# Optimization experiments

Hardware: AMD Instinct MI355X
Metric: run time of the kernel (lower is better)

The kernel has to match this reference:

```python
import jax, jax.numpy as jnp
import numpy as np

N_NODES = 100000
N_EDGES = 1600000
F_IN = 128
HID = 128  # nhid*2
NHID = 64
N_GRAPHS = 512
N_CLASSES = 10
NEG_SLOPE = 0.2  # PyG GATConv default


def setup_inputs() -> dict:
    key = jax.random.key(0)
    ks = jax.random.split(key, 16)
    x = jax.random.normal(ks[0], (N_NODES, F_IN), dtype=jnp.float32)
    edge_index = jax.random.randint(ks[1], (2, N_EDGES), 0, N_NODES, dtype=jnp.int64)
    batch = jnp.sort(jax.random.randint(ks[2], (N_NODES,), 0, N_GRAPHS, dtype=jnp.int64))
    def lin(k, fan_in, shape):
        bound = 1.0 / np.sqrt(fan_in)
        return jax.random.uniform(k, shape, jnp.float32, -bound, bound)
    return {
        "x": x, "edge_index": edge_index, "batch": batch,
        "W1": lin(ks[3], F_IN, (F_IN, HID)),
        "a_src1": lin(ks[4], HID, (HID,)),
        "a_dst1": lin(ks[5], HID, (HID,)),
        "b1": jnp.zeros((HID,), jnp.float32),
        "W2": lin(ks[6], HID, (HID, HID)),
        "a_src2": lin(ks[7], HID, (HID,)),
        "a_dst2": lin(ks[8], HID, (HID,)),
        "b2": jnp.zeros((HID,), jnp.float32),
        "W_fc1": lin(ks[9], HID, (HID, NHID)),
        "b_fc1": lin(ks[10], HID, (NHID,)),
        "W_fc2": lin(ks[11], NHID, (NHID, N_CLASSES)),
        "b_fc2": lin(ks[12], NHID, (N_CLASSES,)),
    }


def gat_conv(x, src, dst, W, a_src, a_dst, b):
    # h = W x ; attention e_ij = LeakyReLU(a_src.h_i + a_dst.h_j), softmax over
    # incoming edges of each destination j, then scatter-add aggregation.
    h = x @ W                                   # [N, H]
    alpha_s = h @ a_src                         # [N]
    alpha_d = h @ a_dst                         # [N]
    e = jax.nn.leaky_relu(alpha_s[src] + alpha_d[dst], NEG_SLOPE)  # [E]
    n = x.shape[0]
    m = jax.ops.segment_max(e, dst, num_segments=n)                # per-dst max
    ex = jnp.exp(e - m[dst])
    denom = jax.ops.segment_sum(ex, dst, num_segments=n)
    alpha = ex / denom[dst]                                        # [E]
    out = jax.ops.segment_sum(alpha[:, None] * h[src], dst, num_segments=n)
    return out + b


def reference(x, edge_index, batch, W1, a_src1, a_dst1, b1,
              W2, a_src2, a_dst2, b2, W_fc1, b_fc1, W_fc2, b_fc2):
    n = x.shape[0]
    # GATConv default add_self_loops=True
    loops = jnp.arange(n, dtype=edge_index.dtype)
    src = jnp.concatenate([edge_index[0], loops])
    dst = jnp.concatenate([edge_index[1], loops])

    h = jax.nn.selu(gat_conv(x, src, dst, W1, a_src1, a_dst1, b1))
    h = jax.nn.selu(gat_conv(h, src, dst, W2, a_src2, a_dst2, b2))

    # global mean pool over graphs
    sums = jax.ops.segment_sum(h, batch, num_segments=N_GRAPHS)
    cnts = jax.ops.segment_sum(jnp.ones((n,), h.dtype), batch, num_segments=N_GRAPHS)
    pooled = jax.nn.selu(sums / jnp.maximum(cnts, 1.0)[:, None])   # [G, H]

    g = jax.nn.selu(pooled @ W_fc1 + b_fc1)
    # dropout p=0.5 is identity in eval mode
    logits = g @ W_fc2 + b_fc2
    return jax.nn.log_softmax(logits, axis=-1)
```

## Files before the change

### kernel.cpp

```cpp
#include <hip/hip_runtime.h>
#include <hip/hip_bf16.h>

#define NEG_SLOPE 0.2f
typedef unsigned int uint32;

#define BSHIFT 9
#define BSIZE 512
#define MAXB 256
#define PCHUNK 4096

typedef __attribute__((ext_vector_type(8))) __bf16 bf16x8;
typedef __attribute__((ext_vector_type(4))) float f32x4;

__device__ __forceinline__ float selu_f(float x) {
    const float a = 1.6732632423543772f, s = 1.0507009873554805f;
    return x > 0.0f ? s * x : s * a * (__expf(x) - 1.0f);
}

__device__ __forceinline__ unsigned short f2bf(float x) {
    uint32 u = __float_as_uint(x);
    uint32 r = (u + 0x7fff + ((u >> 16) & 1)) >> 16;
    return (unsigned short)r;
}
__device__ __forceinline__ float bf_lo(uint32 g) { return __uint_as_float(g << 16); }
__device__ __forceinline__ float bf_hi(uint32 g) { return __uint_as_float(g & 0xffff0000u); }

__global__ __launch_bounds__(256) void prep9(const float* __restrict__ W1,
                                             const float* __restrict__ W2,
                                             unsigned short* __restrict__ Wb,
                                             const int* __restrict__ batch,
                                             int* __restrict__ gstart,
                                             const int* __restrict__ ei,
                                             int* __restrict__ gcnt,
                                             int N, int G, int E, int TOT, int GB) {
    __shared__ int lh[MAXB];
    int b = blockIdx.x, t = threadIdx.x;
    if (b < 2) {
        const float* W = b ? W2 : W1;
        unsigned short* oh = Wb + (size_t)b * 32768;
        unsigned short* ol = oh + 16384;
        for (int d = t; d < 16384; d += 256) {
            int j = d & 7, nn = (d >> 3) & 127, g = d >> 10;
            float v = W[(g * 8 + j) * 128 + nn];
            uint32 hu = f2bf(v);
            float hv = __uint_as_float(hu << 16);
            oh[d] = (unsigned short)hu;
            ol[d] = f2bf(v - hv);
        }
    } else if (b < 2 + GB) {
        int i = (b - 2) * 256 + t;
        if (i < N) {
            int bb = batch[i];
            int bp = (i == 0) ? -1 : batch[i - 1];
            for (int q = bp + 1; q <= bb; ++q) gstart[q] = i;
            if (i == N - 1)
                for (int q = bb + 1; q <= G; ++q) gstart[q] = N;
        }
    } else {
        int hb_ = b - 2 - GB;
        lh[t] = 0;
        __syncthreads();
        int eb = hb_ * PCHUNK;
        #pragma unroll
        for (int k = 0; k < PCHUNK / 256; ++k) {
            int e = eb + k * 256 + t;
            if (e < TOT) {
                int d = (e < E) ? ei[E + e] : e - E;
                atomicAdd(&lh[d >> BSHIFT], 1);
            }
        }
        __syncthreads();
        if (lh[t] > 0) atomicAdd(&gcnt[t], lh[t]);
    }
}

__global__ __launch_bounds__(256) void bucket_scan(const int* __restrict__ gcnt,
                                                   int* __restrict__ bstart,
                                                   int* __restrict__ gcursor, int NB, int TOT) {
    __shared__ int sh[256];
    int t = threadIdx.x;
    int v = (t < NB) ? gcnt[t] : 0;
    sh[t] = v;
    __syncthreads();
    for (int off = 1; off < 256; off <<= 1) {
        int add = (t >= off) ? sh[t - off] : 0;
        __syncthreads();
        sh[t] += add;
        __syncthreads();
    }
    int ex = sh[t] - v;
    if (t < NB) { bstart[t] = ex; gcursor[t] = ex; }
    if (t == 0) bstart[NB] = TOT;
}

__global__ __launch_bounds__(256) void partition_edges(const int* __restrict__ ei,
                                                       int* __restrict__ gcursor,
                                                       uint32* __restrict__ tmp,
                                                       int E, int TOT) {
    __shared__ int lcnt[MAXB];
    __shared__ int lstart[MAXB];
    __shared__ int lcur[MAXB];
    __shared__ int gbase[MAXB];
    __shared__ uint32 staged[PCHUNK];
    __shared__ unsigned char bslot[PCHUNK];
    int t = threadIdx.x;
    int eb = blockIdx.x * PCHUNK;
    int sreg[16], dreg[16];
    #pragma unroll
    for (int k = 0; k < 16; ++k) {
        int e = eb + k * 256 + t;
        if (e < TOT) {
            if (e < E) { sreg[k] = ei[e]; dreg[k] = ei[E + e]; }
            else       { sreg[k] = dreg[k] = e - E; }
        } else dreg[k] = -1;
    }
    lcnt[t] = 0;
    __syncthreads();
    #pragma unroll
    for (int k = 0; k < 16; ++k)
        if (dreg[k] >= 0) atomicAdd(&lcnt[dreg[k] >> BSHIFT], 1);
    __syncthreads();
    int v = lcnt[t];
    lstart[t] = v;
    __syncthreads();
    for (int off = 1; off < 256; off <<= 1) {
        int add = (t >= off) ? lstart[t - off] : 0;
        __syncthreads();
        lstart[t] += add;
        __syncthreads();
    }
    int ex = lstart[t] - v;
    __syncthreads();
    lstart[t] = ex;
    lcur[t] = ex;
    if (v > 0) gbase[t] = atomicAdd(&gcursor[t], v);
    __syncthreads();
    #pragma unroll
    for (int k = 0; k < 16; ++k) {
        int d = dreg[k];
        if (d >= 0) {
            int b = d >> BSHIFT;
            int p = atomicAdd(&lcur[b], 1);
            staged[p] = ((uint32)(d & (BSIZE - 1)) << 17) | (uint32)sreg[k];
            bslot[p] = (unsigned char)b;
        }
    }
    __syncthreads();
    int nvalid = TOT - eb; if (nvalid > PCHUNK) nvalid = PCHUNK;
    for (int i = t; i < nvalid; i += 256) {
        int b = bslot[i];
        tmp[gbase[b] + (i - lstart[b])] = staged[i];
    }
}

__global__ __launch_bounds__(256) void bucket_build(const uint32* __restrict__ tmp,
                                                    const int* __restrict__ bstart,
                                                    int* __restrict__ rowptr,
                                                    int* __restrict__ col,
                                                    int N, int TOT, int NB) {
    __shared__ int cnt[BSIZE];
    __shared__ int sums[256];
    int b = blockIdx.x, t = threadIdx.x;
    int lo = b << BSHIFT;
    int nn = N - lo; if (nn > BSIZE) nn = BSIZE;
    cnt[t] = 0; cnt[t + 256] = 0;
    __syncthreads();
    int ebeg = bstart[b], eend = bstart[b + 1];
    for (int i = ebeg + t; i < eend; i += 256)
        atomicAdd(&cnt[tmp[i] >> 17], 1);
    __syncthreads();
    int c0 = cnt[2 * t], c1 = cnt[2 * t + 1];
    int s2 = c0 + c1;
    sums[t] = s2;
    __syncthreads();
    for (int off = 1; off < 256; off <<= 1) {
        int add = (t >= off) ? sums[t - off] : 0;
        __syncthreads();
        sums[t] += add;
        __syncthreads();
    }
    int ex = sums[t] - s2;
    int st0 = ebeg + ex, st1 = st0 + c0;
    if (2 * t < nn)     rowptr[lo + 2 * t] = st0;
    if (2 * t + 1 < nn) rowptr[lo + 2 * t + 1] = st1;
    cnt[2 * t] = st0; cnt[2 * t + 1] = st1;
    __syncthreads();
    for (int i = ebeg + t; i < eend; i += 256) {
        uint32 u = tmp[i];
        int p = atomicAdd(&cnt[u >> 17], 1);
        col[p] = (int)(u & 0x1FFFFu);
    }
    if (b == NB - 1 && t == 0) rowptr[N] = TOT;
}

__device__ __forceinline__ void gemm_core(const bf16x8 ah[2][4],
                                          const __bf16* Wl,
                                          const float* a_src, const float* a_dst,
                                          uint32* hb, float* as_, float* ad_,
                                          int rbase, int n, int col16, int quad) {
    f32x4 acc[2][8];
    #pragma unroll
    for (int mt = 0; mt < 2; ++mt)
        #pragma unroll
        for (int t = 0; t < 8; ++t) acc[mt][t] = (f32x4)(0.0f);

    #pragma unroll
    for (int c = 0; c < 4; ++c) {
        #pragma unroll
        for (int t = 0; t < 8; ++t) {
            int off = (((c * 4 + quad) * 128) + t * 16 + col16) * 8;
            bf16x8 bh = *(const bf16x8*)&Wl[off];
            bf16x8 bl = *(const bf16x8*)&Wl[16384 + off];
            #pragma unroll
            for (int mt = 0; mt < 2; ++mt) {
                acc[mt][t] = __builtin_amdgcn_mfma_f32_16x16x32_bf16(ah[mt][c], bh, acc[mt][t], 0, 0, 0);
                acc[mt][t] = __builtin_amdgcn_mfma_f32_16x16x32_bf16(ah[mt][c], bl, acc[mt][t], 0, 0, 0);
            }
        }
    }
    float asv[8], adv[8];
    #pragma unroll
    for (int t = 0; t < 8; ++t) { asv[t] = a_src[t * 16 + col16]; adv[t] = a_dst[t * 16 + col16]; }
    #pragma unroll
    for (int mt = 0; mt < 2; ++mt) {
        #pragma unroll
        for (int reg = 0; reg < 4; ++reg) {
            float s = 0.0f, d = 0.0f;
            #pragma unroll
            for (int t = 0; t < 8; ++t) {
                float v = acc[mt][t][reg];
                s += v * asv[t]; d += v * adv[t];
            }
            #pragma unroll
            for (int off = 1; off < 16; off <<= 1) {
                s += __shfl_xor(s, off);
                d += __shfl_xor(d, off);
            }
            int r = rbase + mt * 16 + quad * 4 + reg;
            if (col16 == 0 && r < n) { as_[r] = s; ad_[r] = d; }
        }
    }
    #pragma unroll
    for (int mt = 0; mt < 2; ++mt)
    #pragma unroll
    for (int t = 0; t < 8; ++t)
    #pragma unroll
    for (int reg = 0; reg < 4; ++reg) {
        float v = acc[mt][t][reg];
        float p = __shfl_xor(v, 1);
        int r = rbase + mt * 16 + quad * 4 + reg;
        if (!(col16 & 1) && r < n) {
            uint32 pk = (uint32)f2bf(v) | ((uint32)f2bf(p) << 16);
            hb[(size_t)r * 64 + t * 8 + (col16 >> 1)] = pk;
        }
    }
}

__global__ __launch_bounds__(256) void gemm_mfma_f32(const float* __restrict__ X,
                                                     const unsigned short* __restrict__ Wbh,
                                                     const float* __restrict__ a_src,
                                                     const float* __restrict__ a_dst,
                                                     uint32* __restrict__ hb,
                                                     float* __restrict__ as_,
                                                     float* __restrict__ ad_, int n) {
    __shared__ __bf16 Wl[32768];
    const int tid = threadIdx.x;
    {
        const uint4* sw = (const uint4*)Wbh;
        uint4* dw = (uint4*)Wl;
        for (int i = tid; i < 4096; i += 256) dw[i] = sw[i];
    }
    const int lane = tid & 63, wid = tid >> 6;
    const int col16 = lane & 15, quad = lane >> 4;
    const int rbase = blockIdx.x * 128 + wid * 32;
    bf16x8 ah[2][4];
    #pragma unroll
    for (int mt = 0; mt < 2; ++mt) {
        int r = rbase + mt * 16 + col16;
        bool ok = (r < n);
        const float* xp = X + (size_t)r * 128;
        #pragma unroll
        for (int c = 0; c < 4; ++c) {
            int k0 = c * 32 + quad * 8;
            float4 x0 = ok ? *(const float4*)(xp + k0)     : make_float4(0.f,0.f,0.f,0.f);
            float4 x1 = ok ? *(const float4*)(xp + k0 + 4) : make_float4(0.f,0.f,0.f,0.f);
            float xs[8] = {x0.x,x0.y,x0.z,x0.w,x1.x,x1.y,x1.z,x1.w};
            #pragma unroll
            for (int j = 0; j < 8; ++j) ah[mt][c][j] = (__bf16)xs[j];
        }
    }
    __syncthreads();
    gemm_core(ah, Wl, a_src, a_dst, hb, as_, ad_, rbase, n, col16, quad);
}

__global__ __launch_bounds__(256) void gemm_mfma_bf16(const __bf16* __restrict__ X,
                                                      const unsigned short* __restrict__ Wbh,
                                                      const float* __restrict__ a_src,
                                                      const float* __restrict__ a_dst,
                                                      uint32* __restrict__ hb,
                                                      float* __restrict__ as_,
                                                      float* __restrict__ ad_, int n) {
    __shared__ __bf16 Wl[32768];
    const int tid = threadIdx.x;
    {
        const uint4* sw = (const uint4*)Wbh;
        uint4* dw = (uint4*)Wl;
        for (int i = tid; i < 4096; i += 256) dw[i] = sw[i];
    }
    const int lane = tid & 63, wid = tid >> 6;
    const int col16 = lane & 15, quad = lane >> 4;
    const int rbase = blockIdx.x * 128 + wid * 32;
    bf16x8 ah[2][4];
    const bf16x8 zz = (bf16x8)((__bf16)0.0f);
    #pragma unroll
    for (int mt = 0; mt < 2; ++mt) {
        int r = rbase + mt * 16 + col16;
        bool ok = (r < n);
        const __bf16* xp = X + (size_t)r * 128;
        #pragma unroll
        for (int c = 0; c < 4; ++c)
            ah[mt][c] = ok ? *(const bf16x8*)(xp + c * 32 + quad * 8) : zz;
    }
    __syncthreads();
    gemm_core(ah, Wl, a_src, a_dst, hb, as_, ad_, rbase, n, col16, quad);
}

__global__ __launch_bounds__(256) void gat_csr3(const int* __restrict__ rowptr,
                                                const int* __restrict__ col,
                                                const uint2* __restrict__ hb2,
                                                const float* __restrict__ as_,
                                                const float* __restrict__ ad_,
                                                const float* __restrict__ bias,
                                                uint2* __restrict__ outb, int n) {
    __shared__ float wsh[4][2][32];
    __shared__ int   ssh[4][2][32];
    const int wid = threadIdx.x >> 6;
    const int lane = threadIdx.x & 63;
    const int sub = lane >> 5, l = lane & 31;
    const int node = blockIdx.x * 8 + wid * 2 + sub;
    const bool valid = node < n;
    int beg = 0, end = 0;
    if (valid) { beg = rowptr[node]; end = rowptr[node + 1]; }
    float add = valid ? ad_[node] : 0.0f;
    int deg = end - beg;
    int mdeg = max(deg, __shfl_xor(deg, 32));
    float m = -INFINITY, s = 0.0f;
    float a0 = 0.f, a1 = 0.f, a2 = 0.f, a3 = 0.f;
    for (int cb = 0; cb < mdeg; cb += 32) {
        int j = beg + cb + l;
        bool eok = (j < end);
        int srcn = eok ? col[j] : 0;
        float v = eok ? (as_[srcn] + add) : -INFINITY;
        v = (v > 0.0f) ? v : NEG_SLOPE * v;
        float cm = v;
        #pragma unroll
        for (int off = 16; off > 0; off >>= 1) cm = fmaxf(cm, __shfl_xor(cm, off));
        float nm = fmaxf(m, cm);
        float w = eok ? __expf(v - nm) : 0.0f;
        float ws = w;
        #pragma unroll
        for (int off = 16; off > 0; off >>= 1) ws += __shfl_xor(ws, off);
        float scale = (m == -INFINITY) ? 0.0f : __expf(m - nm);
        s = s * scale + ws;
        a0 *= scale; a1 *= scale; a2 *= scale; a3 *= scale;
        wsh[wid][sub][l] = w;
        ssh[wid][sub][l] = srcn;
        int cnt = end - beg - cb;
        cnt = (cnt > 32) ? 32 : (cnt < 0 ? 0 : cnt);
        int t = 0;
        for (; t + 8 <= cnt; t += 8) {
            int sr[8]; float wr[8]; uint2 g[8];
            #pragma unroll
            for (int q = 0; q < 8; ++q) { sr[q] = ssh[wid][sub][t + q]; wr[q] = wsh[wid][sub][t + q]; }
            #pragma unroll
            for (int q = 0; q < 8; ++q) g[q] = hb2[(uint32)sr[q] * 32u + l];
            #pragma unroll
            for (int q = 0; q < 8; ++q) {
                a0 += wr[q] * bf_lo(g[q].x); a1 += wr[q] * bf_hi(g[q].x);
                a2 += wr[q] * bf_lo(g[q].y); a3 += wr[q] * bf_hi(g[q].y);
            }
        }
        for (; t < cnt; ++t) {
            int sn = ssh[wid][sub][t];
            float wt = wsh[wid][sub][t];
            uint2 g = hb2[(uint32)sn * 32u + l];
            a0 += wt * bf_lo(g.x); a1 += wt * bf_hi(g.x);
            a2 += wt * bf_lo(g.y); a3 += wt * bf_hi(g.y);
        }
        m = nm;
    }
    if (valid) {
        float inv = 1.0f / s;
        float4 bv = *(const float4*)&bias[l * 4];
        float r0 = selu_f(a0 * inv + bv.x);
        float r1 = selu_f(a1 * inv + bv.y);
        float r2 = selu_f(a2 * inv + bv.z);
        float r3 = selu_f(a3 * inv + bv.w);
        uint2 o;
        o.x = (uint32)f2bf(r0) | ((uint32)f2bf(r1) << 16);
        o.y = (uint32)f2bf(r2) | ((uint32)f2bf(r3) << 16);
        outb[(uint32)node * 32u + l] = o;
    }
}

__global__ __launch_bounds__(128) void pool_head(const uint32* __restrict__ act,
                                                 const int* __restrict__ gstart,
                                                 const float* __restrict__ Wfc1,
                                                 const float* __restrict__ bfc1,
                                                 const float* __restrict__ Wfc2,
                                                 const float* __restrict__ bfc2,
                                                 float* __restrict__ out) {
    __shared__ float part[128][2];
    __shared__ float p[128];
    __shared__ float q[64];
    __shared__ float l[10];
    __shared__ float red[2];
    int g = blockIdx.x, t = threadIdx.x;
    int lo = gstart[g], hi = gstart[g + 1];
    int half = t >> 6, u = t & 63;
    float acc0 = 0.f, acc1 = 0.f;
    for (int nd = lo + half; nd < hi; nd += 2) {
        uint32 gv = act[(uint32)nd * 64u + u];
        acc0 += bf_lo(gv); acc1 += bf_hi(gv);
    }
    part[t][0] = acc0; part[t][1] = acc1;
    __syncthreads();
    if (half == 0) {
        float c = fmaxf((float)(hi - lo), 1.0f);
        p[2 * u]     = selu_f((acc0 + part[t + 64][0]) / c);
        p[2 * u + 1] = selu_f((acc1 + part[t + 64][1]) / c);
    }
    __syncthreads();
    if (t < 64) {
        float a = bfc1[t];
        #pragma unroll 8
        for (int k = 0; k < 128; ++k) a += p[k] * Wfc1[k * 64 + t];
        q[t] = selu_f(a);
    }
    __syncthreads();
    if (t < 10) {
        float a = bfc2[t];
        #pragma unroll
        for (int k = 0; k < 64; ++k) a += q[k] * Wfc2[k * 10 + t];
        l[t] = a;
    }
    __syncthreads();
    if (t == 0) {
        float mx = l[0];
        for (int c = 1; c < 10; ++c) mx = fmaxf(mx, l[c]);
        float sum = 0.0f;
        for (int c = 0; c < 10; ++c) sum += __expf(l[c] - mx);
        red[0] = mx; red[1] = logf(sum);
    }
    __syncthreads();
    if (t < 10) out[g * 10 + t] = l[t] - red[0] - red[1];
}

extern "C" void kernel_launch(void* const* d_in, const int* in_sizes, int n_in,
                              void* d_out, int out_size, void* d_ws, size_t ws_size,
                              hipStream_t stream) {
    const float* x      = (const float*)d_in[0];
    const int*   ei     = (const int*)d_in[1];
    const int*   batch  = (const int*)d_in[2];
    const float* W1     = (const float*)d_in[3];
    const float* asrc1  = (const float*)d_in[4];
    const float* adst1  = (const float*)d_in[5];
    const float* b1     = (const float*)d_in[6];
    const float* W2     = (const float*)d_in[7];
    const float* asrc2  = (const float*)d_in[8];
    const float* adst2  = (const float*)d_in[9];
    const float* b2     = (const float*)d_in[10];
    const float* Wfc1   = (const float*)d_in[11];
    const float* bfc1   = (const float*)d_in[12];
    const float* Wfc2   = (const float*)d_in[13];
    const float* bfc2   = (const float*)d_in[14];
    float* out = (float*)d_out;

    const int N = in_sizes[0] / 128;
    const int E = in_sizes[1] / 2;
    const int G = out_size / 10;
    const int TOT = E + N;
    const int NB = ((N - 1) >> BSHIFT) + 1;
    const int GB = (N + 255) / 256;
    const int PH = (TOT + PCHUNK - 1) / PCHUNK;

    uint32* hb    = (uint32*)d_ws;
    uint32* h2b   = hb + (size_t)N * 64;
    uint32* tmp   = h2b + (size_t)N * 64;
    float* as_    = (float*)(tmp + TOT);
    float* ad_    = as_ + N;
    int*   gstart = (int*)(ad_ + N);
    int*   rowptr = gstart + (G + 2);
    int*   gcnt   = rowptr + (N + 2);
    int*   bstart = gcnt + MAXB;
    int*   gcursor= bstart + MAXB + 1;
    int*   col    = gcursor + MAXB;
    unsigned short* Wb = (unsigned short*)(((uintptr_t)(col + TOT) + 255) & ~(uintptr_t)255);

    const int gemmGrid = (N + 127) / 128;
    const int gatGrid  = (N + 7) / 8;

    hipMemsetAsync(gcnt, 0, MAXB * 4, stream);
    prep9<<<2 + GB + PH, 256, 0, stream>>>(W1, W2, Wb, batch, gstart, ei, gcnt,
                                           N, G, E, TOT, GB);
    bucket_scan<<<1, 256, 0, stream>>>(gcnt, bstart, gcursor, NB, TOT);
    partition_edges<<<PH, 256, 0, stream>>>(ei, gcursor, tmp, E, TOT);
    bucket_build<<<NB, 256, 0, stream>>>(tmp, bstart, rowptr, col, N, TOT, NB);

    gemm_mfma_f32<<<gemmGrid, 256, 0, stream>>>(x, Wb, asrc1, adst1, hb, as_, ad_, N);
    gat_csr3<<<gatGrid, 256, 0, stream>>>(rowptr, col, (const uint2*)hb, as_, ad_, b1, (uint2*)h2b, N);

    gemm_mfma_bf16<<<gemmGrid, 256, 0, stream>>>((const __bf16*)h2b, Wb + 32768, asrc2, adst2, hb, as_, ad_, N);
    gat_csr3<<<gatGrid, 256, 0, stream>>>(rowptr, col, (const uint2*)hb, as_, ad_, b2, (uint2*)h2b, N);

    pool_head<<<G, 128, 0, stream>>>(h2b, gstart, Wfc1, bfc1, Wfc2, bfc2, out);
}
```

Before: 403.9 us.

## Fuse layer-1 GEMM with prep kernel and fold bucket scan into consumers

Merges the W1 bf16 split, the layer-1 MFMA GEMM, graph-start computation, and the edge bucket histogram into one heterogeneous launch. Each GEMM block converts W1 directly into shared memory instead of reading a pre-split copy. The separate bucket_scan kernel is removed, and partition_edges and bucket_build each recompute the prefix scan of bucket counts locally. This saves launches and dependency bubbles at the cost of redundant W1 conversion per block and repeated small scans.

```diff
diff --git a/kernel.cpp b/kernel.cpp
--- a/kernel.cpp
+++ b/kernel.cpp
@@ -25,30 +25,119 @@
 __device__ __forceinline__ float bf_lo(uint32 g) { return __uint_as_float(g << 16); }
 __device__ __forceinline__ float bf_hi(uint32 g) { return __uint_as_float(g & 0xffff0000u); }
 
-__global__ __launch_bounds__(256) void prep9(const float* __restrict__ W1,
-                                             const float* __restrict__ W2,
-                                             unsigned short* __restrict__ Wb,
-                                             const int* __restrict__ batch,
-                                             int* __restrict__ gstart,
-                                             const int* __restrict__ ei,
-                                             int* __restrict__ gcnt,
-                                             int N, int G, int E, int TOT, int GB) {
-    __shared__ int lh[MAXB];
+__device__ __forceinline__ void gemm_core(const bf16x8 ah[2][4],
+                                          const __bf16* Wl,
+                                          const float* a_src, const float* a_dst,
+                                          uint32* hb, float* as_, float* ad_,
+                                          int rbase, int n, int col16, int quad) {
+    f32x4 acc[2][8];
+    #pragma unroll
+    for (int mt = 0; mt < 2; ++mt)
+        #pragma unroll
+        for (int t = 0; t < 8; ++t) acc[mt][t] = (f32x4)(0.0f);
+
+    #pragma unroll
+    for (int c = 0; c < 4; ++c) {
+        #pragma unroll
+        for (int t = 0; t < 8; ++t) {
+            int off = (((c * 4 + quad) * 128) + t * 16 + col16) * 8;
+            bf16x8 bh = *(const bf16x8*)&Wl[off];
+            bf16x8 bl = *(const bf16x8*)&Wl[16384 + off];
+            #pragma unroll
+            for (int mt = 0; mt < 2; ++mt) {
+                acc[mt][t] = __builtin_amdgcn_mfma_f32_16x16x32_bf16(ah[mt][c], bh, acc[mt][t], 0, 0, 0);
+                acc[mt][t] = __builtin_amdgcn_mfma_f32_16x16x32_bf16(ah[mt][c], bl, acc[mt][t], 0, 0, 0);
+            }
+        }
+    }
+    float asv[8], adv[8];
+    #pragma unroll
+    for (int t = 0; t < 8; ++t) { asv[t] = a_src[t * 16 + col16]; adv[t] = a_dst[t * 16 + col16]; }
+    #pragma unroll
+    for (int mt = 0; mt < 2; ++mt) {
+        #pragma unroll
+        for (int reg = 0; reg < 4; ++reg) {
+            float s = 0.0f, d = 0.0f;
+            #pragma unroll
+            for (int t = 0; t < 8; ++t) {
+                float v = acc[mt][t][reg];
+                s += v * asv[t]; d += v * adv[t];
+            }
+            #pragma unroll
+            for (int off = 1; off < 16; off <<= 1) {
+                s += __shfl_xor(s, off);
+                d += __shfl_xor(d, off);
+            }
+            int r = rbase + mt * 16 + quad * 4 + reg;
+            if (col16 == 0 && r < n) { as_[r] = s; ad_[r] = d; }
+        }
+    }
+    #pragma unroll
+    for (int mt = 0; mt < 2; ++mt)
+    #pragma unroll
+    for (int t = 0; t < 8; ++t)
+    #pragma unroll
+    for (int reg = 0; reg < 4; ++reg) {
+        float v = acc[mt][t][reg];
+        float p = __shfl_xor(v, 1);
+        int r = rbase + mt * 16 + quad * 4 + reg;
+        if (!(col16 & 1) && r < n) {
+            uint32 pk = (uint32)f2bf(v) | ((uint32)f2bf(p) << 16);
+            hb[(size_t)r * 64 + t * 8 + (col16 >> 1)] = pk;
+        }
+    }
+}
+
+__global__ __launch_bounds__(256) void fused1(const float* __restrict__ X,
+                                              const float* __restrict__ W1,
+                                              const float* __restrict__ W2,
+                                              unsigned short* __restrict__ Wb,
+                                              const float* __restrict__ asrc1,
+                                              const float* __restrict__ adst1,
+                                              uint32* __restrict__ hb,
+                                              float* __restrict__ as_,
+                                              float* __restrict__ ad_,
+                                              const int* __restrict__ batch,
+                                              int* __restrict__ gstart,
+                                              const int* __restrict__ ei,
+                                              int* __restrict__ gcnt,
+                                              int N, int G, int E, int TOT,
+                                              int GemmG, int GB) {
+    __shared__ __bf16 Wl[32768];
     int b = blockIdx.x, t = threadIdx.x;
-    if (b < 2) {
-        const float* W = b ? W2 : W1;
-        unsigned short* oh = Wb + (size_t)b * 32768;
-        unsigned short* ol = oh + 16384;
+    if (b < GemmG) {
+        unsigned short* Wls = (unsigned short*)Wl;
         for (int d = t; d < 16384; d += 256) {
             int j = d & 7, nn = (d >> 3) & 127, g = d >> 10;
-            float v = W[(g * 8 + j) * 128 + nn];
+            float v = W1[(g * 8 + j) * 128 + nn];
             uint32 hu = f2bf(v);
             float hv = __uint_as_float(hu << 16);
-            oh[d] = (unsigned short)hu;
-            ol[d] = f2bf(v - hv);
-        }
-    } else if (b < 2 + GB) {
-        int i = (b - 2) * 256 + t;
+            Wls[d] = (unsigned short)hu;
+            Wls[16384 + d] = f2bf(v - hv);
+        }
+        const int lane = t & 63, wid = t >> 6;
+        const int col16 = lane & 15, quad = lane >> 4;
+        const int rbase = b * 128 + wid * 32;
+        bf16x8 ah[2][4];
+        #pragma unroll
+        for (int mt = 0; mt < 2; ++mt) {
+            int r = rbase + mt * 16 + col16;
+            bool ok = (r < N);
+            const float* xp = X + (size_t)r * 128;
+            #pragma unroll
+            for (int c = 0; c < 4; ++c) {
+                int k0 = c * 32 + quad * 8;
+                float4 x0 = ok ? *(const float4*)(xp + k0)     : make_float4(0.f,0.f,0.f,0.f);
+                float4 x1 = ok ? *(const float4*)(xp + k0 + 4) : make_float4(0.f,0.f,0.f,0.f);
+                float xs[8] = {x0.x,x0.y,x0.z,x0.w,x1.x,x1.y,x1.z,x1.w};
+                #pragma unroll
+                for (int j = 0; j < 8; ++j) ah[mt][c][j] = (__bf16)xs[j];
+            }
+        }
+        __syncthreads();
+        gemm_core(ah, Wl, asrc1, adst1, hb, as_, ad_, rbase, N, col16, quad);
+    } else if (b < GemmG + GB) {
+        int i = (b - GemmG) * 256 + t;
         if (i < N) {
             int bb = batch[i];
             int bp = (i == 0) ? -1 : batch[i - 1];
@@ -56,8 +145,9 @@
             if (i == N - 1)
                 for (int q = bb + 1; q <= G; ++q) gstart[q] = N;
         }
-    } else {
-        int hb_ = b - 2 - GB;
+    } else if (b < GemmG + GB + ((TOT + PCHUNK - 1) / PCHUNK)) {
+        int* lh = (int*)Wl;
+        int hb_ = b - GemmG - GB;
         lh[t] = 0;
         __syncthreads();
         int eb = hb_ * PCHUNK;
@@ -71,36 +161,28 @@
         }
         __syncthreads();
         if (lh[t] > 0) atomicAdd(&gcnt[t], lh[t]);
-    }
-}
-
-__global__ __launch_bounds__(256) void bucket_scan(const int* __restrict__ gcnt,
-                                                   int* __restrict__ bstart,
-                                                   int* __restrict__ gcursor, int NB, int TOT) {
-    __shared__ int sh[256];
-    int t = threadIdx.x;
-    int v = (t < NB) ? gcnt[t] : 0;
-    sh[t] = v;
-    __syncthreads();
-    for (int off = 1; off < 256; off <<= 1) {
-        int add = (t >= off) ? sh[t - off] : 0;
-        __syncthreads();
-        sh[t] += add;
-        __syncthreads();
-    }
-    int ex = sh[t] - v;
-    if (t < NB) { bstart[t] = ex; gcursor[t] = ex; }
-    if (t == 0) bstart[NB] = TOT;
+    } else {
+        for (int d = t; d < 16384; d += 256) {
+            int j = d & 7, nn = (d >> 3) & 127, g = d >> 10;
+            float v = W2[(g * 8 + j) * 128 + nn];
+            uint32 hu = f2bf(v);
+            float hv = __uint_as_float(hu << 16);
+            Wb[d] = (unsigned short)hu;
+            Wb[16384 + d] = f2bf(v - hv);
+        }
+    }
 }
 
 __global__ __launch_bounds__(256) void partition_edges(const int* __restrict__ ei,
-                                                       int* __restrict__ gcursor,
+                                                       const int* __restrict__ gcnt,
+                                                       int* __restrict__ gcur0,
                                                        uint32* __restrict__ tmp,
-                                                       int E, int TOT) {
+                                                       int E, int TOT, int NB) {
     __shared__ int lcnt[MAXB];
     __shared__ int lstart[MAXB];
     __shared__ int lcur[MAXB];
     __shared__ int gbase[MAXB];
+    __shared__ int gs[MAXB];
     __shared__ uint32 staged[PCHUNK];
     __shared__ unsigned char bslot[PCHUNK];
     int t = threadIdx.x;
@@ -115,6 +197,8 @@
         } else dreg[k] = -1;
     }
     lcnt[t] = 0;
+    int gv = (t < NB) ? gcnt[t] : 0;
+    gs[t] = gv;
     __syncthreads();
     #pragma unroll
     for (int k = 0; k < 16; ++k)
@@ -124,16 +208,19 @@
     lstart[t] = v;
     __syncthreads();
     for (int off = 1; off < 256; off <<= 1) {
-        int add = (t >= off) ? lstart[t - off] : 0;
-        __syncthreads();
-        lstart[t] += add;
+        int addL = (t >= off) ? lstart[t - off] : 0;
+        int addG = (t >= off) ? gs[t - off] : 0;
+        __syncthreads();
+        lstart[t] += addL;
+        gs[t] += addG;
         __syncthreads();
     }
     int ex = lstart[t] - v;
+    int gex = gs[t] - gv;
     __syncthreads();
     lstart[t] = ex;
     lcur[t] = ex;
-    if (v > 0) gbase[t] = atomicAdd(&gcursor[t], v);
+    if (v > 0) gbase[t] = gex + atomicAdd(&gcur0[t], v);
     __syncthreads();
     #pragma unroll
     for (int k = 0; k < 16; ++k) {
@@ -154,18 +241,30 @@
 }
 
 __global__ __launch_bounds__(256) void bucket_build(const uint32* __restrict__ tmp,
-                                                    const int* __restrict__ bstart,
+                                                    const int* __restrict__ gcnt,
                                                     int* __restrict__ rowptr,
                                                     int* __restrict__ col,
                                                     int N, int TOT, int NB) {
     __shared__ int cnt[BSIZE];
     __shared__ int sums[256];
+    __shared__ int gs[256];
+    __shared__ int eb2[2];
     int b = blockIdx.x, t = threadIdx.x;
     int lo = b << BSHIFT;
     int nn = N - lo; if (nn > BSIZE) nn = BSIZE;
     cnt[t] = 0; cnt[t + 256] = 0;
-    __syncthreads();
-    int ebeg = bstart[b], eend = bstart[b + 1];
+    int gv = (t < NB) ? gcnt[t] : 0;
+    gs[t] = gv;
+    __syncthreads();
+    for (int off = 1; off < 256; off <<= 1) {
+        int add = (t >= off) ? gs[t - off] : 0;
+        __syncthreads();
+        gs[t] += add;
+        __syncthreads();
+    }
+    if (t == b) { eb2[0] = gs[t] - gv; eb2[1] = gs[t]; }
+    __syncthreads();
+    int ebeg = eb2[0], eend = eb2[1];
     for (int i = ebeg + t; i < eend; i += 256)
         atomicAdd(&cnt[tmp[i] >> 17], 1);
     __syncthreads();
@@ -191,106 +290,6 @@
         col[p] = (int)(u & 0x1FFFFu);
     }
     if (b == NB - 1 && t == 0) rowptr[N] = TOT;
-}
-
-__device__ __forceinline__ void gemm_core(const bf16x8 ah[2][4],
-                                          const __bf16* Wl,
-                                          const float* a_src, const float* a_dst,
-                                          uint32* hb, float* as_, float* ad_,
-                                          int rbase, int n, int col16, int quad) {
-    f32x4 acc[2][8];
-    #pragma unroll
-    for (int mt = 0; mt < 2; ++mt)
-        #pragma unroll
-        for (int t = 0; t < 8; ++t) acc[mt][t] = (f32x4)(0.0f);
-
-    #pragma unroll
-    for (int c = 0; c < 4; ++c) {
-        #pragma unroll
-        for (int t = 0; t < 8; ++t) {
-            int off = (((c * 4 + quad) * 128) + t * 16 + col16) * 8;
-            bf16x8 bh = *(const bf16x8*)&Wl[off];
-            bf16x8 bl = *(const bf16x8*)&Wl[16384 + off];
-            #pragma unroll
-            for (int mt = 0; mt < 2; ++mt) {
-                acc[mt][t] = __builtin_amdgcn_mfma_f32_16x16x32_bf16(ah[mt][c], bh, acc[mt][t], 0, 0, 0);
-                acc[mt][t] = __builtin_amdgcn_mfma_f32_16x16x32_bf16(ah[mt][c], bl, acc[mt][t], 0, 0, 0);
-            }
-        }
-    }
-    float asv[8], adv[8];
-    #pragma unroll
-    for (int t = 0; t < 8; ++t) { asv[t] = a_src[t * 16 + col16]; adv[t] = a_dst[t * 16 + col16]; }
-    #pragma unroll
-    for (int mt = 0; mt < 2; ++mt) {
-        #pragma unroll
-        for (int reg = 0; reg < 4; ++reg) {
-            float s = 0.0f, d = 0.0f;
-            #pragma unroll
-            for (int t = 0; t < 8; ++t) {
-                float v = acc[mt][t][reg];
-                s += v * asv[t]; d += v * adv[t];
-            }
-            #pragma unroll
-            for (int off = 1; off < 16; off <<= 1) {
-                s += __shfl_xor(s, off);
-                d += __shfl_xor(d, off);
-            }
-            int r = rbase + mt * 16 + quad * 4 + reg;
-            if (col16 == 0 && r < n) { as_[r] = s; ad_[r] = d; }
-        }
-    }
-    #pragma unroll
-    for (int mt = 0; mt < 2; ++mt)
-    #pragma unroll
-    for (int t = 0; t < 8; ++t)
-    #pragma unroll
-    for (int reg = 0; reg < 4; ++reg) {
-        float v = acc[mt][t][reg];
-        float p = __shfl_xor(v, 1);
-        int r = rbase + mt * 16 + quad * 4 + reg;
-        if (!(col16 & 1) && r < n) {
-            uint32 pk = (uint32)f2bf(v) | ((uint32)f2bf(p) << 16);
-            hb[(size_t)r * 64 + t * 8 + (col16 >> 1)] = pk;
-        }
-    }
-}
-
-__global__ __launch_bounds__(256) void gemm_mfma_f32(const float* __restrict__ X,
-                                                     const unsigned short* __restrict__ Wbh,
-                                                     const float* __restrict__ a_src,
-                                                     const float* __restrict__ a_dst,
-                                                     uint32* __restrict__ hb,
-                                                     float* __restrict__ as_,
-                                                     float* __restrict__ ad_, int n) {
-    __shared__ __bf16 Wl[32768];
-    const int tid = threadIdx.x;
-    {
-        const uint4* sw = (const uint4*)Wbh;
-        uint4* dw = (uint4*)Wl;
-        for (int i = tid; i < 4096; i += 256) dw[i] = sw[i];
-    }
-    const int lane = tid & 63, wid = tid >> 6;
-    const int col16 = lane & 15, quad = lane >> 4;
-    const int rbase = blockIdx.x * 128 + wid * 32;
-    bf16x8 ah[2][4];
-    #pragma unroll
-    for (int mt = 0; mt < 2; ++mt) {
-        int r = rbase + mt * 16 + col16;
-        bool ok = (r < n);
-        const float* xp = X + (size_t)r * 128;
-        #pragma unroll
-        for (int c = 0; c < 4; ++c) {
-            int k0 = c * 32 + quad * 8;
-            float4 x0 = ok ? *(const float4*)(xp + k0)     : make_float4(0.f,0.f,0.f,0.f);
-            float4 x1 = ok ? *(const float4*)(xp + k0 + 4) : make_float4(0.f,0.f,0.f,0.f);
-            float xs[8] = {x0.x,x0.y,x0.z,x0.w,x1.x,x1.y,x1.z,x1.w};
-            #pragma unroll
-            for (int j = 0; j < 8; ++j) ah[mt][c][j] = (__bf16)xs[j];
-        }
-    }
-    __syncthreads();
-    gemm_core(ah, Wl, a_src, a_dst, hb, as_, ad_, rbase, n, col16, quad);
 }
 
 __global__ __launch_bounds__(256) void gemm_mfma_bf16(const __bf16* __restrict__ X,
@@ -483,6 +482,7 @@
     const int NB = ((N - 1) >> BSHIFT) + 1;
     const int GB = (N + 255) / 256;
     const int PH = (TOT + PCHUNK - 1) / PCHUNK;
+    const int GemmG = (N + 127) / 128;
 
     uint32* hb    = (uint32*)d_ws;
     uint32* h2b   = hb + (size_t)N * 64;
@@ -492,25 +492,22 @@
     int*   gstart = (int*)(ad_ + N);
     int*   rowptr = gstart + (G + 2);
     int*   gcnt   = rowptr + (N + 2);
-    int*   bstart = gcnt + MAXB;
-    int*   gcursor= bstart + MAXB + 1;
-    int*   col    = gcursor + MAXB;
+    int*   gcur0  = gcnt + MAXB;
+    int*   col    = gcur0 + MAXB;
     unsigned short* Wb = (unsigned short*)(((uintptr_t)(col + TOT) + 255) & ~(uintptr_t)255);
 
-    const int gemmGrid = (N + 127) / 128;
-    const int gatGrid  = (N + 7) / 8;
-
-    hipMemsetAsync(gcnt, 0, MAXB * 4, stream);
-    prep9<<<2 + GB + PH, 256, 0, stream>>>(W1, W2, Wb, batch, gstart, ei, gcnt,
-                                           N, G, E, TOT, GB);
-    bucket_scan<<<1, 256, 0, stream>>>(gcnt, bstart, gcursor, NB, TOT);
-    partition_edges<<<PH, 256, 0, stream>>>(ei, gcursor, tmp, E, TOT);
-    bucket_build<<<NB, 256, 0, stream>>>(tmp, bstart, rowptr, col, N, TOT, NB);
-
-    gemm_mfma_f32<<<gemmGrid, 256, 0, stream>>>(x, Wb, asrc1, adst1, hb, as_, ad_, N);
+    const int gatGrid = (N + 7) / 8;
+
+    hipMemsetAsync(gcnt, 0, 2 * MAXB * 4, stream);
+    fused1<<<GemmG + GB + PH + 1, 256, 0, stream>>>(x, W1, W2, Wb, asrc1, adst1,
+                                                    hb, as_, ad_, batch, gstart,
+                                                    ei, gcnt, N, G, E, TOT, GemmG, GB);
+    partition_edges<<<PH, 256, 0, stream>>>(ei, gcnt, gcur0, tmp, E, TOT, NB);
+    bucket_build<<<NB, 256, 0, stream>>>(tmp, gcnt, rowptr, col, N, TOT, NB);
+
     gat_csr3<<<gatGrid, 256, 0, stream>>>(rowptr, col, (const uint2*)hb, as_, ad_, b1, (uint2*)h2b, N);
 
-    gemm_mfma_bf16<<<gemmGrid, 256, 0, stream>>>((const __bf16*)h2b, Wb + 32768, asrc2, adst2, hb, as_, ad_, N);
+    gemm_mfma_bf16<<<GemmG, 256, 0, stream>>>((const __bf16*)h2b, Wb, asrc2, adst2, hb, as_, ad_, N);
     gat_csr3<<<gatGrid, 256, 0, stream>>>(rowptr, col, (const uint2*)hb, as_, ad_, b2, (uint2*)h2b, N);
 
     pool_head<<<G, 128, 0, stream>>>(h2b, gstart, Wfc1, bfc1, Wfc2, bfc2, out);
```

New measurement: 402.5 us. Within noise of the previous version (-0.4%).
